# Optimization experiments

Measured on AMD Instinct MI355X. Metric: run time of the kernel, lower is better.

## Reference

```python
import jax, jax.numpy as jnp
import numpy as np


def _compute_features(ff):
    # ff: (..., 4) = [rx, ry, rvx, rvy]
    rx, ry, rvx, rvy = ff[..., 0], ff[..., 1], ff[..., 2], ff[..., 3]
    dist_sq = rx * rx + ry * ry
    dist = jnp.sqrt(dist_sq + 1e-06)
    inv_dist = 1.0 / (dist + 0.1)
    dir_x = rx / (dist + 1e-06)
    dir_y = ry / (dist + 1e-06)
    speed_sq = rvx * rvx + rvy * rvy
    rel_speed = jnp.sqrt(speed_sq + 1e-06)
    dot_vp = rvx * rx + rvy * ry
    closing_speed = dot_vp / (dist + 1e-06)
    ttca = jnp.tanh(-dot_vp / (speed_sq + 1e-06))
    return jnp.stack(
        [rx, ry, rvx, rvy, dist, inv_dist, rel_speed, closing_speed,
         dir_x, dir_y, ttca, dot_vp], axis=-1)  # (..., 12)


def setup_inputs() -> dict:
    key = jax.random.key(0)
    k0, k1, k2, k3, k4 = jax.random.split(key, 5)
    B, N, H, HID, IN = 16, 256, 8, 64, 12
    ff = jax.random.normal(k0, (B, N, N, 4), dtype=jnp.float32)
    # nn.Linear default init scale ~ 1/sqrt(fan_in); use small random weights
    W1 = jax.random.normal(k1, (IN, HID), dtype=jnp.float32) / np.sqrt(IN)
    b1 = jax.random.normal(k2, (HID,), dtype=jnp.float32) / np.sqrt(IN)
    W2 = jax.random.normal(k3, (HID, H), dtype=jnp.float32) / np.sqrt(HID)
    b2 = jax.random.normal(k4, (H,), dtype=jnp.float32) / np.sqrt(HID)
    return {"fundamental_features": ff, "W1": W1, "b1": b1, "W2": W2, "b2": b2}


def reference(fundamental_features, W1, b1, W2, b2):
    feats = _compute_features(fundamental_features)          # (B, N, N, 12)
    h = jax.nn.silu(jnp.einsum('bnmf,fh->bnmh', feats, W1) + b1)  # (B, N, N, 64)
    bias = jnp.einsum('bnmh,ho->bnmo', h, W2) + b2            # (B, N, N, H)
    return jnp.transpose(bias, (0, 3, 1, 2))                  # (B, H, N, N)
```

## Files before the change

### kernel.cpp

```cpp
#include <hip/hip_runtime.h>
#include <hip/hip_bf16.h>

#define NH 8
#define HID 64
#define NPAIRS (16 * 256 * 256)
#define BLOCK 256
#define GPW 8
#define LSTR 68

typedef __attribute__((ext_vector_type(8))) short bf16x8;
typedef __attribute__((ext_vector_type(4))) float f32x4;

union F8 { bf16x8 v; unsigned u[4]; uint4 q4; };

__device__ __host__ inline unsigned bfpk(float a, float b) {
    unsigned ua = __float_as_uint(a); ua += 0x7fffu + ((ua >> 16) & 1u);
    unsigned ub = __float_as_uint(b); ub += 0x7fffu + ((ub >> 16) & 1u);
    return (ua >> 16) | (ub & 0xffff0000u);
}

__global__ void pack_weights(const float* __restrict__ W1, const float* __restrict__ b1,
                             const float* __restrict__ W2, const float* __restrict__ b2,
                             unsigned char* __restrict__ ws) {
    int l = threadIdx.x;
    int n = l & 15, q = l >> 4;
    unsigned* B1 = (unsigned*)ws;
    unsigned* B2 = (unsigned*)(ws + 4096);
    float* b1v = (float*)(ws + 6144);
    float* b2v = (float*)(ws + 7168);
    for (int nb = 0; nb < 4; ++nb) {
        int h = nb * 16 + n;
        for (int j2 = 0; j2 < 4; ++j2) {
            int k0 = q * 8 + 2 * j2;
            float v0 = (k0 < 12) ? W1[k0 * HID + h] : 0.f;
            float v1 = (k0 + 1 < 12) ? W1[(k0 + 1) * HID + h] : 0.f;
            B1[(nb * 64 + l) * 4 + j2] = bfpk(v0, v1);
        }
        b1v[nb * 64 + l] = b1[h];
    }
    for (int kc = 0; kc < 2; ++kc)
        for (int j2 = 0; j2 < 4; ++j2) {
            int k0 = kc * 32 + q * 8 + 2 * j2;
            float v0 = (n < NH) ? W2[k0 * NH + n] : 0.f;
            float v1 = (n < NH) ? W2[(k0 + 1) * NH + n] : 0.f;
            B2[(kc * 64 + l) * 4 + j2] = bfpk(v0, v1);
        }
    b2v[l] = (n < NH) ? b2[n] : 0.f;
}

__global__ __launch_bounds__(BLOCK) void relfeat_mfma(
    const float* __restrict__ ff, const unsigned char* __restrict__ ws,
    float* __restrict__ out)
{
    __shared__ float lds[4][16 * LSTR];
    const int tid = threadIdx.x;
    const int w = tid >> 6, l = tid & 63;
    const int n = l & 15, q = l >> 4;
    float* my = lds[w];

    F8 B1[4]; F8 B2[2];
    const uint4* B1p = (const uint4*)ws;
    const uint4* B2p = (const uint4*)(ws + 4096);
    #pragma unroll
    for (int nb = 0; nb < 4; ++nb) B1[nb].q4 = B1p[nb * 64 + l];
    #pragma unroll
    for (int kc = 0; kc < 2; ++kc) B2[kc].q4 = B2p[kc * 64 + l];
    float b1v[4];
    #pragma unroll
    for (int nb = 0; nb < 4; ++nb) b1v[nb] = ((const float*)(ws + 6144))[nb * 64 + l];
    const float b2v = ((const float*)(ws + 7168))[l];

    const int wave_base = (blockIdx.x * 4 + w) * (GPW * 16);

    for (int g = 0; g < GPW; ++g) {
        const int pbase = wave_base + g * 16;

        F8 a1; a1.u[0] = a1.u[1] = a1.u[2] = a1.u[3] = 0u;
        if (q < 2) {
            float4 v = ((const float4*)ff)[pbase + n];
            float rx = v.x, ry = v.y, rvx = v.z, rvy = v.w;
            float dist_sq = rx * rx + ry * ry;
            float dist = sqrtf(dist_sq + 1e-6f);
            float speed_sq = rvx * rvx + rvy * rvy;
            float dot_vp = rvx * rx + rvy * ry;
            float invd = __builtin_amdgcn_rcpf(dist + 1e-6f);
            if (q == 0) {
                float inv_dist = __builtin_amdgcn_rcpf(dist + 0.1f);
                float rel_speed = sqrtf(speed_sq + 1e-6f);
                float closing = dot_vp * invd;
                a1.u[0] = bfpk(rx, ry);
                a1.u[1] = bfpk(rvx, rvy);
                a1.u[2] = bfpk(dist, inv_dist);
                a1.u[3] = bfpk(rel_speed, closing);
            } else {
                float dir_x = rx * invd, dir_y = ry * invd;
                float z = -dot_vp * __builtin_amdgcn_rcpf(speed_sq + 1e-6f);
                float ez = __expf(2.f * z);
                float ttca = 1.f - 2.f * __builtin_amdgcn_rcpf(ez + 1.f);
                a1.u[0] = bfpk(dir_x, dir_y);
                a1.u[1] = bfpk(ttca, dot_vp);
            }
        }

        #pragma unroll
        for (int nb = 0; nb < 4; ++nb) {
            f32x4 d1 = {0.f, 0.f, 0.f, 0.f};
            d1 = __builtin_amdgcn_mfma_f32_16x16x32_bf16(a1.v, B1[nb].v, d1, 0, 0, 0);
            #pragma unroll
            for (int r = 0; r < 4; ++r) {
                float x = d1[r] + b1v[nb];
                float s = x * __builtin_amdgcn_rcpf(1.f + __expf(-x));
                my[(q * 4 + r) * LSTR + nb * 16 + n] = s;
            }
        }

        f32x4 d2 = {b2v, b2v, b2v, b2v};
        #pragma unroll
        for (int kc = 0; kc < 2; ++kc) {
            const float* rp = &my[n * LSTR + kc * 32 + q * 8];
            float4 lo = *(const float4*)rp;
            float4 hi = *(const float4*)(rp + 4);
            F8 a2;
            a2.u[0] = bfpk(lo.x, lo.y); a2.u[1] = bfpk(lo.z, lo.w);
            a2.u[2] = bfpk(hi.x, hi.y); a2.u[3] = bfpk(hi.z, hi.w);
            d2 = __builtin_amdgcn_mfma_f32_16x16x32_bf16(a2.v, B2[kc].v, d2, 0, 0, 0);
        }

        if (n < NH) {
            int p0 = pbase + q * 4;
            int b = p0 >> 16, lo16 = p0 & 65535;
            float4 st; st.x = d2[0]; st.y = d2[1]; st.z = d2[2]; st.w = d2[3];
            *(float4*)(out + (size_t)b * (NH * 65536) + (size_t)n * 65536 + lo16) = st;
        }
    }
}

extern "C" void kernel_launch(void* const* d_in, const int* in_sizes, int n_in,
                              void* d_out, int out_size, void* d_ws, size_t ws_size,
                              hipStream_t stream) {
    const float* ff = (const float*)d_in[0];
    const float* W1 = (const float*)d_in[1];
    const float* b1 = (const float*)d_in[2];
    const float* W2 = (const float*)d_in[3];
    const float* b2 = (const float*)d_in[4];
    float* out = (float*)d_out;
    unsigned char* ws = (unsigned char*)d_ws;

    pack_weights<<<1, 64, 0, stream>>>(W1, b1, W2, b2, ws);
    const int grid = NPAIRS / (16 * GPW * 4);
    relfeat_mfma<<<grid, BLOCK, 0, stream>>>(ff, ws, out);
}
```

Before: 114.4 us.

## Switch first layer to 32x32x16 MFMA with bias folded into accumulator

```diff
diff --git a/kernel.cpp b/kernel.cpp
--- a/kernel.cpp
+++ b/kernel.cpp
@@ -1,15 +1,15 @@
 #include <hip/hip_runtime.h>
-#include <hip/hip_bf16.h>
 
 #define NH 8
 #define HID 64
 #define NPAIRS (16 * 256 * 256)
 #define BLOCK 256
-#define GPW 8
+#define GPW 4
 #define LSTR 68
 
 typedef __attribute__((ext_vector_type(8))) short bf16x8;
 typedef __attribute__((ext_vector_type(4))) float f32x4;
+typedef __attribute__((ext_vector_type(16))) float f32x16;
 
 union F8 { bf16x8 v; unsigned u[4]; uint4 q4; };
 
@@ -23,114 +23,116 @@
                              const float* __restrict__ W2, const float* __restrict__ b2,
                              unsigned char* __restrict__ ws) {
     int l = threadIdx.x;
-    int n = l & 15, q = l >> 4;
+    int n32 = l & 31, q2 = l >> 5;
+    int n16 = l & 15, q4 = l >> 4;
     unsigned* B1 = (unsigned*)ws;
-    unsigned* B2 = (unsigned*)(ws + 4096);
-    float* b1v = (float*)(ws + 6144);
-    float* b2v = (float*)(ws + 7168);
-    for (int nb = 0; nb < 4; ++nb) {
-        int h = nb * 16 + n;
+    unsigned* B2 = (unsigned*)(ws + 2048);
+    float* b1v = (float*)(ws + 4096);
+    float* b2v = (float*)(ws + 4608);
+    for (int m = 0; m < 2; ++m) {
+        int h = m * 32 + n32;
         for (int j2 = 0; j2 < 4; ++j2) {
-            int k0 = q * 8 + 2 * j2;
+            int k0 = q2 * 8 + 2 * j2;
             float v0 = (k0 < 12) ? W1[k0 * HID + h] : 0.f;
             float v1 = (k0 + 1 < 12) ? W1[(k0 + 1) * HID + h] : 0.f;
-            B1[(nb * 64 + l) * 4 + j2] = bfpk(v0, v1);
+            B1[(m * 64 + l) * 4 + j2] = bfpk(v0, v1);
         }
-        b1v[nb * 64 + l] = b1[h];
+        b1v[m * 64 + l] = b1[h];
     }
     for (int kc = 0; kc < 2; ++kc)
         for (int j2 = 0; j2 < 4; ++j2) {
-            int k0 = kc * 32 + q * 8 + 2 * j2;
-            float v0 = (n < NH) ? W2[k0 * NH + n] : 0.f;
-            float v1 = (n < NH) ? W2[(k0 + 1) * NH + n] : 0.f;
+            int k0 = kc * 32 + q4 * 8 + 2 * j2;
+            float v0 = (n16 < NH) ? W2[k0 * NH + n16] : 0.f;
+            float v1 = (n16 < NH) ? W2[(k0 + 1) * NH + n16] : 0.f;
             B2[(kc * 64 + l) * 4 + j2] = bfpk(v0, v1);
         }
-    b2v[l] = (n < NH) ? b2[n] : 0.f;
+    b2v[l] = (n16 < NH) ? b2[n16] : 0.f;
 }
 
-__global__ __launch_bounds__(BLOCK) void relfeat_mfma(
+__global__ __launch_bounds__(BLOCK) void relfeat_mfma2(
     const float* __restrict__ ff, const unsigned char* __restrict__ ws,
     float* __restrict__ out)
 {
-    __shared__ float lds[4][16 * LSTR];
+    __shared__ float lds[4][32 * LSTR];
     const int tid = threadIdx.x;
     const int w = tid >> 6, l = tid & 63;
-    const int n = l & 15, q = l >> 4;
+    const int n32 = l & 31, q2 = l >> 5;
+    const int n16 = l & 15, q4 = l >> 4;
     float* my = lds[w];
 
-    F8 B1[4]; F8 B2[2];
-    const uint4* B1p = (const uint4*)ws;
-    const uint4* B2p = (const uint4*)(ws + 4096);
+    F8 B1f[2], B2f[2];
     #pragma unroll
-    for (int nb = 0; nb < 4; ++nb) B1[nb].q4 = B1p[nb * 64 + l];
+    for (int m = 0; m < 2; ++m)  B1f[m].q4 = ((const uint4*)ws)[m * 64 + l];
     #pragma unroll
-    for (int kc = 0; kc < 2; ++kc) B2[kc].q4 = B2p[kc * 64 + l];
-    float b1v[4];
+    for (int kc = 0; kc < 2; ++kc) B2f[kc].q4 = ((const uint4*)(ws + 2048))[kc * 64 + l];
+    float b1s[2];
+    b1s[0] = ((const float*)(ws + 4096))[l];
+    b1s[1] = ((const float*)(ws + 4096))[64 + l];
+    const float b2s = ((const float*)(ws + 4608))[l];
+
+    f32x16 cbias[2];
     #pragma unroll
-    for (int nb = 0; nb < 4; ++nb) b1v[nb] = ((const float*)(ws + 6144))[nb * 64 + l];
-    const float b2v = ((const float*)(ws + 7168))[l];
+    for (int m = 0; m < 2; ++m)
+        #pragma unroll
+        for (int r = 0; r < 16; ++r) cbias[m][r] = b1s[m];
 
-    const int wave_base = (blockIdx.x * 4 + w) * (GPW * 16);
+    const int wave_base = (blockIdx.x * 4 + w) * (GPW * 32);
 
     for (int g = 0; g < GPW; ++g) {
-        const int pbase = wave_base + g * 16;
+        const int pbase = wave_base + g * 32;
 
-        F8 a1; a1.u[0] = a1.u[1] = a1.u[2] = a1.u[3] = 0u;
-        if (q < 2) {
-            float4 v = ((const float4*)ff)[pbase + n];
-            float rx = v.x, ry = v.y, rvx = v.z, rvy = v.w;
-            float dist_sq = rx * rx + ry * ry;
-            float dist = sqrtf(dist_sq + 1e-6f);
-            float speed_sq = rvx * rvx + rvy * rvy;
-            float dot_vp = rvx * rx + rvy * ry;
-            float invd = __builtin_amdgcn_rcpf(dist + 1e-6f);
-            if (q == 0) {
-                float inv_dist = __builtin_amdgcn_rcpf(dist + 0.1f);
-                float rel_speed = sqrtf(speed_sq + 1e-6f);
-                float closing = dot_vp * invd;
-                a1.u[0] = bfpk(rx, ry);
-                a1.u[1] = bfpk(rvx, rvy);
-                a1.u[2] = bfpk(dist, inv_dist);
-                a1.u[3] = bfpk(rel_speed, closing);
-            } else {
-                float dir_x = rx * invd, dir_y = ry * invd;
-                float z = -dot_vp * __builtin_amdgcn_rcpf(speed_sq + 1e-6f);
-                float ez = __expf(2.f * z);
-                float ttca = 1.f - 2.f * __builtin_amdgcn_rcpf(ez + 1.f);
-                a1.u[0] = bfpk(dir_x, dir_y);
-                a1.u[1] = bfpk(ttca, dot_vp);
+        float4 v = ((const float4*)ff)[pbase + n32];
+        float rx = v.x, ry = v.y, rvx = v.z, rvy = v.w;
+        float dist_sq = rx * rx + ry * ry;
+        float dist = sqrtf(dist_sq + 1e-6f);
+        float speed_sq = rvx * rvx + rvy * rvy;
+        float dot_vp = rvx * rx + rvy * ry;
+        float invd = __builtin_amdgcn_rcpf(dist + 1e-6f);
+        float inv_dist = __builtin_amdgcn_rcpf(dist + 0.1f);
+        float rel_speed = sqrtf(speed_sq + 1e-6f);
+        float closing = dot_vp * invd;
+        float dir_x = rx * invd, dir_y = ry * invd;
+        float z = -dot_vp * __builtin_amdgcn_rcpf(speed_sq + 1e-6f);
+        float ez = __expf(2.f * z);
+        float ttca = 1.f - 2.f * __builtin_amdgcn_rcpf(ez + 1.f);
+
+        F8 a1;
+        a1.u[0] = (q2 == 0) ? bfpk(rx, ry)          : bfpk(dir_x, dir_y);
+        a1.u[1] = (q2 == 0) ? bfpk(rvx, rvy)        : bfpk(ttca, dot_vp);
+        a1.u[2] = (q2 == 0) ? bfpk(dist, inv_dist)  : 0u;
+        a1.u[3] = (q2 == 0) ? bfpk(rel_speed, closing) : 0u;
+
+        #pragma unroll
+        for (int m = 0; m < 2; ++m) {
+            f32x16 d1 = __builtin_amdgcn_mfma_f32_32x32x16_bf16(a1.v, B1f[m].v, cbias[m], 0, 0, 0);
+            #pragma unroll
+            for (int r = 0; r < 16; ++r) {
+                int prow = (r & 3) + 8 * (r >> 2) + 4 * q2;
+                float x = d1[r];
+                float s = x * __builtin_amdgcn_rcpf(1.f + __expf(-x));
+                my[prow * LSTR + m * 32 + n32] = s;
             }
         }
 
         #pragma unroll
-        for (int nb = 0; nb < 4; ++nb) {
-            f32x4 d1 = {0.f, 0.f, 0.f, 0.f};
-            d1 = __builtin_amdgcn_mfma_f32_16x16x32_bf16(a1.v, B1[nb].v, d1, 0, 0, 0);
+        for (int hl = 0; hl < 2; ++hl) {
+            f32x4 d2 = {b2s, b2s, b2s, b2s};
             #pragma unroll
-            for (int r = 0; r < 4; ++r) {
-                float x = d1[r] + b1v[nb];
-                float s = x * __builtin_amdgcn_rcpf(1.f + __expf(-x));
-                my[(q * 4 + r) * LSTR + nb * 16 + n] = s;
+            for (int kc = 0; kc < 2; ++kc) {
+                const float* rp = &my[(hl * 16 + n16) * LSTR + kc * 32 + q4 * 8];
+                float4 lo = *(const float4*)rp;
+                float4 hi = *(const float4*)(rp + 4);
+                F8 a2;
+                a2.u[0] = bfpk(lo.x, lo.y); a2.u[1] = bfpk(lo.z, lo.w);
+                a2.u[2] = bfpk(hi.x, hi.y); a2.u[3] = bfpk(hi.z, hi.w);
+                d2 = __builtin_amdgcn_mfma_f32_16x16x32_bf16(a2.v, B2f[kc].v, d2, 0, 0, 0);
             }
-        }
-
-        f32x4 d2 = {b2v, b2v, b2v, b2v};
-        #pragma unroll
-        for (int kc = 0; kc < 2; ++kc) {
-            const float* rp = &my[n * LSTR + kc * 32 + q * 8];
-            float4 lo = *(const float4*)rp;
-            float4 hi = *(const float4*)(rp + 4);
-            F8 a2;
-            a2.u[0] = bfpk(lo.x, lo.y); a2.u[1] = bfpk(lo.z, lo.w);
-            a2.u[2] = bfpk(hi.x, hi.y); a2.u[3] = bfpk(hi.z, hi.w);
-            d2 = __builtin_amdgcn_mfma_f32_16x16x32_bf16(a2.v, B2[kc].v, d2, 0, 0, 0);
-        }
-
-        if (n < NH) {
-            int p0 = pbase + q * 4;
-            int b = p0 >> 16, lo16 = p0 & 65535;
-            float4 st; st.x = d2[0]; st.y = d2[1]; st.z = d2[2]; st.w = d2[3];
-            *(float4*)(out + (size_t)b * (NH * 65536) + (size_t)n * 65536 + lo16) = st;
+            if (n16 < NH) {
+                int p0 = pbase + hl * 16 + q4 * 4;
+                int b = p0 >> 16, lo16 = p0 & 65535;
+                float4 st; st.x = d2[0]; st.y = d2[1]; st.z = d2[2]; st.w = d2[3];
+                *(float4*)(out + (size_t)b * (NH * 65536) + (size_t)n16 * 65536 + lo16) = st;
+            }
         }
     }
 }
@@ -147,6 +149,6 @@
     unsigned char* ws = (unsigned char*)d_ws;
 
     pack_weights<<<1, 64, 0, stream>>>(W1, b1, W2, b2, ws);
-    const int grid = NPAIRS / (16 * GPW * 4);
-    relfeat_mfma<<<grid, BLOCK, 0, stream>>>(ff, ws, out);
+    const int grid = NPAIRS / (32 * GPW * 4);
+    relfeat_mfma2<<<grid, BLOCK, 0, stream>>>(ff, ws, out);
 }
```

Result: faster. 104.8 us (-8.4%).
